# Optimization experiments

Measured on AMD Instinct MI355X. Metric: run time of the kernel, lower is better.

## Reference

```python
import jax, jax.numpy as jnp
import numpy as np
import math

B, S, D, H = 1, 2048, 2048, 16
DH, DHID, DKER = 128, 256, 128  # dim_head, dim_hid, dim_ker


def _uniform(k, shape, a):
    return jax.random.uniform(k, shape, jnp.float32, -a, a)


def setup_inputs() -> dict:
    key = jax.random.key(0)
    ks = jax.random.split(key, 14)
    a1 = math.sqrt(6.0 / (DH + DHID))
    a2 = math.sqrt(6.0 / (DKER + DHID))
    a3 = math.sqrt(6.0 / (2 * DKER))
    return {
        "x_t": jax.random.normal(ks[0], (B, S, D), jnp.float32),
        "q": jax.random.normal(ks[1], (B, S, D), jnp.float32),
        "k": jax.random.normal(ks[2], (B, S, D), jnp.float32),
        "v": jax.random.normal(ks[3], (B, S, D), jnp.float32),
        "lr_attn_mask": jax.random.bernoulli(ks[4], 0.5, (B, H, S, S)),
        "sparse_norms_lse": jax.random.normal(ks[5], (B, H, S, 1), jnp.float32),
        "sparse_attn_weights": jax.random.normal(ks[6], (B, H, S, S), jnp.float32),
        "lambda_constant": 0,
        "kernel_q_mat1": _uniform(ks[7], (H, DH, DHID), a1),
        "kernel_k_mat1": _uniform(ks[8], (H, DH, DHID), a1),
        "kernel_q_mat2": _uniform(ks[9], (H, DHID, DKER), a2),
        "kernel_k_mat2": _uniform(ks[10], (H, DHID, DKER), a2),
        "interaction_k": _uniform(ks[11], (H, DKER, DKER), a3),
        "scalingD": jnp.full((1, H, 1, DKER), 1e-4, jnp.float32),
        "scalingD2": jnp.full((1, H, 1, DKER), 1e-4, jnp.float32),
    }


def _gelu(x):
    return jax.nn.gelu(x, approximate=False)  # matches torch F.gelu default


def reference(x_t, q, k, v, lr_attn_mask, sparse_norms_lse, sparse_attn_weights,
              lambda_constant, kernel_q_mat1, kernel_k_mat1, kernel_q_mat2,
              kernel_k_mat2, interaction_k, scalingD, scalingD2):
    Bq, Sq, Dq = q.shape
    dh = Dq // H
    # [B,S,D] -> [B,H,S,dh]
    qh = q.reshape(Bq, Sq, H, dh).transpose(0, 2, 1, 3)
    kh = k.reshape(Bq, Sq, H, dh).transpose(0, 2, 1, 3)
    vh = v.reshape(Bq, Sq, H, dh).transpose(0, 2, 1, 3)

    # per-head two-layer feature maps (dropout is identity at eval)
    qf = _gelu(jnp.einsum('bhsd,hde->bhse', qh, kernel_q_mat1))
    qf = _gelu(jnp.einsum('bhse,hef->bhsf', qf, kernel_q_mat2))
    kf = _gelu(jnp.einsum('bhsd,hde->bhse', kh, kernel_k_mat1))
    kf = jnp.abs(scalingD) * _gelu(jnp.einsum('bhse,hef->bhsf', kf, kernel_k_mat2))
    kf = kf + jnp.einsum('bhse,hef->bhsf', kf, interaction_k) * scalingD2

    # masked non-negative kernel scores [B,H,S,S]
    scores = jnp.einsum('bhse,bhte->bhst', jnp.abs(qf), jnp.abs(kf))
    m = lr_attn_mask.astype(scores.dtype)
    scores = m * scores

    lr_norms_lse = jnp.log(scores.sum(axis=-1, keepdims=True) + 1e-6)
    norm_factor_lse = jnp.logaddexp(lr_norms_lse, sparse_norms_lse)

    logits = jnp.log(scores + 1e-6) * m + (1.0 - m) * sparse_attn_weights
    attn = jnp.exp(logits - norm_factor_lse)

    out = jnp.einsum('bhst,bhtd->bhsd', attn, vh)
    return out.transpose(0, 2, 1, 3).reshape(Bq, Sq, Dq)
```

## Files before the change

### kernel.cpp

```cpp
#include <hip/hip_runtime.h>
#include <hip/hip_bf16.h>
#include <math.h>

#define H_    16
#define S_    2048
#define D_    2048
#define DH_   128
#define DHID_ 256
#define DKER_ 128

typedef __attribute__((ext_vector_type(8))) short short8v;
typedef __attribute__((ext_vector_type(4))) float float4v;
typedef __attribute__((ext_vector_type(4))) int int4v;

static __device__ __forceinline__ short f2bf(float x){
  union { float f; unsigned u; } v; v.f = x;
  unsigned r = v.u + 0x7fffu + ((v.u >> 16) & 1u);
  return (short)(r >> 16);
}
static __device__ __forceinline__ float gelu_f(float x){
  float y = 0.7978845608028654f * (x + 0.044715f * x * x * x);
  float e = __expf(2.0f * y);
  float t = 1.0f - 2.0f / (e + 1.0f);
  return 0.5f * x * (1.0f + t);
}
static __device__ __forceinline__ float4v mfma16(short8v a, short8v b, float4v c){
  return __builtin_amdgcn_mfma_f32_16x16x32_bf16(a, b, c, 0, 0, 0);
}
static __device__ __forceinline__ unsigned cvtpk(float lo, float hi){
  unsigned d;
  asm("v_cvt_pk_bf16_f32 %0, %1, %2" : "=v"(d) : "v"(lo), "v"(hi));
  return d;
}
static __device__ __forceinline__ void glds16(const void* g, void* l){
  __builtin_amdgcn_global_load_lds(
      (const __attribute__((address_space(1))) void*)g,
      (__attribute__((address_space(3))) void*)l, 16, 0, 0);
}

__global__ __launch_bounds__(256) void prep_kernel(
    const float* __restrict__ w1q, short* __restrict__ W1qT,
    const float* __restrict__ w1k, short* __restrict__ W1kT,
    const float* __restrict__ w2q, short* __restrict__ W2qT,
    const float* __restrict__ w2k, short* __restrict__ W2kT,
    const float* __restrict__ ik,  short* __restrict__ IKT,
    const float* __restrict__ v,   short* __restrict__ V2){
  __shared__ float tile[32][33];
  int b = blockIdx.x;
  int tid = threadIdx.x;

  if (b < 2048){
    int h = b >> 7, bx = b & 127;
    int d = tid & 127, oct = tid >> 7;
    int t8 = bx * 2 + oct;
    int t32 = t8 >> 2, o = t8 & 3;
    const float* src = v + (size_t)(t32 * 32) * D_ + h * DH_ + d;
    short8v ov;
    #pragma unroll
    for (int j = 0; j < 8; ++j){
      int trel = o * 4 + (j & 3) + ((j >> 2) << 4);
      ov[j] = f2bf(src[(size_t)trel * D_]);
    }
    *(short8v*)(V2 + (((size_t)h * (S_/8) + t8) * DH_ + d) * 8) = ov;
    return;
  }
  b -= 2048;
  const float* src; short* dst; int R, C, bx, by, h;
  if (b < 512){        src = w1q; dst = W1qT; R = DH_;  C = DHID_;
                       bx = b & 7; by = (b >> 3) & 3; h = b >> 5; }
  else if (b < 1024){  b -= 512;  src = w1k; dst = W1kT; R = DH_;  C = DHID_;
                       bx = b & 7; by = (b >> 3) & 3; h = b >> 5; }
  else if (b < 1536){  b -= 1024; src = w2q; dst = W2qT; R = DHID_; C = DKER_;
                       bx = b & 3; by = (b >> 2) & 7; h = b >> 5; }
  else if (b < 2048){  b -= 1536; src = w2k; dst = W2kT; R = DHID_; C = DKER_;
                       bx = b & 3; by = (b >> 2) & 7; h = b >> 5; }
  else {               b -= 2048; src = ik;  dst = IKT;  R = DKER_; C = DKER_;
                       bx = b & 3; by = (b >> 2) & 3; h = b >> 4; }
  int tx = tid & 31, ty = tid >> 5;
  int c0 = bx * 32, r0 = by * 32;
  const float* s = src + (size_t)h * R * C;
  short* d = dst + (size_t)h * R * C;
  #pragma unroll
  for (int i = 0; i < 32; i += 8)
    tile[ty + i][tx] = s[(size_t)(r0 + ty + i) * C + (c0 + tx)];
  __syncthreads();
  #pragma unroll
  for (int i = 0; i < 32; i += 8)
    d[(size_t)(c0 + ty + i) * R + (r0 + tx)] = f2bf(tile[tx][ty + i]);
}

__global__ __launch_bounds__(256) void feat_kernel(
    const float* __restrict__ q, const float* __restrict__ k,
    const short* __restrict__ W1qT, const short* __restrict__ W2qT,
    const short* __restrict__ W1kT, const short* __restrict__ W2kT,
    const short* __restrict__ IKT, const float* __restrict__ sD,
    const float* __restrict__ sD2,
    short* __restrict__ QF, short* __restrict__ KF){
  __shared__ __align__(16) short yls[4][16][264];
  int z = blockIdx.y;
  bool isq = z < 16;
  int h = z & 15;
  const float* X = isq ? q : k;
  const short* W1T = isq ? W1qT : W1kT;
  const short* W2T = isq ? W2qT : W2kT;
  int lane = threadIdx.x & 63, warp = threadIdx.x >> 6;
  int s0 = (blockIdx.x * 4 + warp) * 16;
  int col = lane & 15, rg = lane >> 4;
  short8v a[4];
  {
    const float* xr = X + (size_t)(s0 + col) * D_ + h * DH_;
    #pragma unroll
    for (int kb = 0; kb < 4; ++kb){
      int k0 = kb * 32 + rg * 8;
      float4v x0 = *(const float4v*)(xr + k0);
      float4v x1 = *(const float4v*)(xr + k0 + 4);
      union { unsigned u[4]; short8v v8; } t;
      t.u[0] = cvtpk(x0[0], x0[1]); t.u[1] = cvtpk(x0[2], x0[3]);
      t.u[2] = cvtpk(x1[0], x1[1]); t.u[3] = cvtpk(x1[2], x1[3]);
      a[kb] = t.v8;
    }
  }
  const short* wbase = W1T + (size_t)h * DHID_ * DH_;
  #pragma unroll
  for (int j = 0; j < 16; ++j){
    int n = j * 16;
    float4v c = {0.f, 0.f, 0.f, 0.f};
    const short* wr = wbase + (size_t)(n + col) * DH_ + rg * 8;
    #pragma unroll
    for (int kb = 0; kb < 4; ++kb)
      c = mfma16(a[kb], *(const short8v*)(wr + kb * 32), c);
    #pragma unroll
    for (int r = 0; r < 4; ++r)
      yls[warp][rg * 4 + r][n + col] = f2bf(gelu_f(c[r]));
  }
  short8v a2[8];
  #pragma unroll
  for (int kb = 0; kb < 8; ++kb)
    a2[kb] = *(const short8v*)(&yls[warp][col][kb * 32 + rg * 8]);
  const short* wb2 = W2T + (size_t)h * DKER_ * DHID_;

  if (isq){
    short* qb = QF + ((size_t)h * S_ + s0) * DKER_;
    #pragma unroll
    for (int j = 0; j < 8; ++j){
      int n = j * 16;
      float4v c = {0.f, 0.f, 0.f, 0.f};
      const short* wr = wb2 + (size_t)(n + col) * DHID_ + rg * 8;
      #pragma unroll
      for (int kb = 0; kb < 8; ++kb)
        c = mfma16(a2[kb], *(const short8v*)(wr + kb * 32), c);
      #pragma unroll
      for (int r = 0; r < 4; ++r)
        qb[(size_t)(rg * 4 + r) * DKER_ + n + col] = f2bf(fabsf(gelu_f(c[r])));
    }
    return;
  }
  float kf0[8][4];
  #pragma unroll
  for (int j = 0; j < 8; ++j){
    int n = j * 16;
    float4v c = {0.f, 0.f, 0.f, 0.f};
    const short* wr = wb2 + (size_t)(n + col) * DHID_ + rg * 8;
    #pragma unroll
    for (int kb = 0; kb < 8; ++kb)
      c = mfma16(a2[kb], *(const short8v*)(wr + kb * 32), c);
    float sc = fabsf(sD[h * DKER_ + n + col]);
    #pragma unroll
    for (int r = 0; r < 4; ++r) kf0[j][r] = sc * gelu_f(c[r]);
  }
  #pragma unroll
  for (int j = 0; j < 8; ++j)
    #pragma unroll
    for (int r = 0; r < 4; ++r)
      yls[warp][rg * 4 + r][j * 16 + col] = f2bf(kf0[j][r]);
  short8v pa[4];
  #pragma unroll
  for (int kb = 0; kb < 4; ++kb)
    pa[kb] = *(const short8v*)(&yls[warp][col][kb * 32 + rg * 8]);
  const short* ib = IKT + (size_t)h * DKER_ * DKER_;
  short* ko = KF + ((size_t)h * S_ + s0) * DKER_;
  #pragma unroll
  for (int j = 0; j < 8; ++j){
    int n = j * 16;
    float4v c = {0.f, 0.f, 0.f, 0.f};
    const short* ir = ib + (size_t)(n + col) * DKER_ + rg * 8;
    #pragma unroll
    for (int kb = 0; kb < 4; ++kb)
      c = mfma16(pa[kb], *(const short8v*)(ir + kb * 32), c);
    float s2 = sD2[h * DKER_ + n + col];
    #pragma unroll
    for (int r = 0; r < 4; ++r)
      ko[(size_t)(rg * 4 + r) * DKER_ + n + col] = f2bf(fabsf(kf0[j][r] + c[r] * s2));
  }
}

template<int MT>
static __device__ __forceinline__ void attn_tloop(
    const char* __restrict__ mrow0, const float* __restrict__ swrow,
    const char* __restrict__ kf_base, const char* __restrict__ v2_base,
    short* kbuf, short* vbuf,
    int kg0, int kg1, int vg0, int vg1, int lds_lo, int lds_hi,
    int swz, int rowb0, int rg, int col,
    const short8v (&qa)[4], float4v (&acc)[8], float& rs){
  const int NITER = (S_ / 2) / 32;
  for (int ti = 0; ti < NITER; ++ti){
    int cur = ti & 1;
    if (ti + 1 < NITER){
      const char* kt = kf_base + (size_t)(ti + 1) * 8192;
      const char* vt = v2_base + (size_t)(ti + 1) * 8192;
      glds16(kt + kg0, &kbuf[(cur ^ 1) * 4096 + lds_lo]);
      glds16(kt + kg1, &kbuf[(cur ^ 1) * 4096 + lds_hi]);
      glds16(vt + vg0, &vbuf[(cur ^ 1) * 4096 + lds_lo]);
      glds16(vt + vg1, &vbuf[(cur ^ 1) * 4096 + lds_hi]);
    }
    const char* kbp = (const char*)kbuf + cur * 8192;
    const char* vbp = (const char*)vbuf + cur * 8192;

    float4v q0 = {0.f,0.f,0.f,0.f}, q1 = {0.f,0.f,0.f,0.f};
    #pragma unroll
    for (int kk = 0; kk < 4; ++kk){
      short8v a0 = *(const short8v*)(kbp + ((rowb0 + kk * 64) ^ swz));
      short8v a1 = *(const short8v*)(kbp + ((rowb0 + 4096 + kk * 64) ^ swz));
      q0 = mfma16(a0, qa[kk], q0);
      q1 = mfma16(a1, qa[kk], q1);
    }

    const float* swp = swrow + ti * 32;
    float4v sv0 = *(const float4v*)swp;
    float4v sv1 = *(const float4v*)(swp + 16);

    bool m0[4], m1[4];
    if constexpr (MT == 0){
      const int* mp = (const int*)(mrow0 + (size_t)ti * 128);
      int4v x0 = *(const int4v*)mp;
      int4v x1 = *(const int4v*)(mp + 16);
      #pragma unroll
      for (int r = 0; r < 4; ++r){ m0[r] = x0[r] != 0; m1[r] = x1[r] != 0; }
    } else if constexpr (MT == 1){
      const unsigned* mp = (const unsigned*)(mrow0 + (size_t)ti * 32);
      unsigned x0 = mp[0], x1 = mp[4];
      #pragma unroll
      for (int r = 0; r < 4; ++r){
        m0[r] = ((x0 >> (8*r)) & 0xffu) != 0u;
        m1[r] = ((x1 >> (8*r)) & 0xffu) != 0u;
      }
    } else if constexpr (MT == 2){
      const float* mp = (const float*)(mrow0 + (size_t)ti * 128);
      float4v x0 = *(const float4v*)mp;
      float4v x1 = *(const float4v*)(mp + 16);
      #pragma unroll
      for (int r = 0; r < 4; ++r){ m0[r] = x0[r] != 0.0f; m1[r] = x1[r] != 0.0f; }
    } else {
      const int* mp = (const int*)(mrow0 + (size_t)ti * 256);
      int4v xa = *(const int4v*)mp;
      int4v xb = *(const int4v*)(mp + 4);
      int4v xc = *(const int4v*)(mp + 32);
      int4v xd = *(const int4v*)(mp + 36);
      m0[0] = xa[0] != 0; m0[1] = xa[2] != 0; m0[2] = xb[0] != 0; m0[3] = xb[2] != 0;
      m1[0] = xc[0] != 0; m1[1] = xc[2] != 0; m1[2] = xd[0] != 0; m1[3] = xd[2] != 0;
    }

    float p0[4], p1[4];
    #pragma unroll
    for (int r = 0; r < 4; ++r){
      p0[r] = m0[r] ? (q0[r] + 1e-6f) : __expf(sv0[r]);
      p1[r] = m1[r] ? (q1[r] + 1e-6f) : __expf(sv1[r]);
      if (m0[r]) rs += q0[r];
      if (m1[r]) rs += q1[r];
    }
    union { unsigned u[4]; short8v v8; } pw;
    pw.u[0] = cvtpk(p0[0], p0[1]); pw.u[1] = cvtpk(p0[2], p0[3]);
    pw.u[2] = cvtpk(p1[0], p1[1]); pw.u[3] = cvtpk(p1[2], p1[3]);
    short8v pa = pw.v8;

    #pragma unroll
    for (int j = 0; j < 8; ++j){
      short8v vf = *(const short8v*)(vbp + rg * 2048 + (j * 16 + col) * 16);
      acc[j] = mfma16(pa, vf, acc[j]);
    }
    __syncthreads();
  }
}

__global__ __launch_bounds__(512, 4) void main_attn_kernel(
    const short* __restrict__ QF, const short* __restrict__ KF,
    const short* __restrict__ V2, const void* __restrict__ MSK,
    const float* __restrict__ SW, const float* __restrict__ LSE,
    float* __restrict__ OUT){
  __shared__ __align__(16) char smem[65536];
  int tid = threadIdx.x;
  int lane = tid & 63, warp = tid >> 6;
  int hf = warp >> 2, w4 = warp & 3;
  int flat = blockIdx.y * 32 + blockIdx.x;
  int nf = (flat & 7) * 64 + (flat >> 3);
  int sblk = nf & 31, h = nf >> 5;
  int tbase = hf * (S_ / 2);
  int s0 = (sblk * 4 + w4) * 16;
  int col = lane & 15, rg = lane >> 4;

  short* kbuf = (short*)(smem + hf * 32768);
  short* vbuf = (short*)(smem + hf * 32768 + 16384);

  short8v qa[4];
  const short* qr = QF + ((size_t)h * S_ + s0 + col) * DKER_ + rg * 8;
  #pragma unroll
  for (int kb = 0; kb < 4; ++kb) qa[kb] = *(const short8v*)(qr + kb * 32);

  float4v acc[8];
  #pragma unroll
  for (int j = 0; j < 8; ++j) acc[j] = (float4v){0.f, 0.f, 0.f, 0.f};
  float rs = 0.f;

  const char* kf_base = (const char*)(KF + ((size_t)h * S_ + tbase) * DKER_);
  const char* v2_base = (const char*)(V2 + ((size_t)h * (S_/8) + (tbase >> 3)) * DH_ * 8);
  int c0 = w4 * 64 + lane, c1 = c0 + 256;
  int kg0 = (c0 * 16) ^ (((c0 >> 4) & 7) << 4);
  int kg1 = (c1 * 16) ^ (((c1 >> 4) & 7) << 4);
  int vg0 = c0 * 16, vg1 = c1 * 16;
  int lds_lo = w4 * 512, lds_hi = 2048 + w4 * 512;

  const float* swrow = SW + ((size_t)h * S_ + s0 + col) * S_ + tbase + rg * 4;

  glds16(kf_base + kg0, &kbuf[lds_lo]);
  glds16(kf_base + kg1, &kbuf[lds_hi]);
  glds16(v2_base + vg0, &vbuf[lds_lo]);
  glds16(v2_base + vg1, &vbuf[lds_hi]);

  int flag;
  {
    const unsigned* mw = (const unsigned*)MSK;
    int bin = 1, f32ok = 1, odd0 = 1;
    #pragma unroll
    for (int i = 0; i < 16; ++i){
      unsigned w = mw[lane + i * 64];
      if (w > 1u) bin = 0;
      if (w != 0u && w != 0x3F800000u) f32ok = 0;
      if (((lane + i * 64) & 1) && w != 0u) odd0 = 0;
    }
    bin = __all(bin); odd0 = __all(odd0); f32ok = __all(f32ok);
    flag = bin ? (odd0 ? 3 : 0) : (f32ok ? 2 : 1);
  }
  __syncthreads();

  int swz = (col & 7) << 4;
  int rowb0 = col * 256 + rg * 16;
  size_t e0 = ((size_t)h * S_ + s0 + col) * S_ + tbase + rg * 4;

  if (flag == 0)
    attn_tloop<0>((const char*)MSK + e0 * 4, swrow, kf_base, v2_base, kbuf, vbuf,
                  kg0, kg1, vg0, vg1, lds_lo, lds_hi, swz, rowb0, rg, col, qa, acc, rs);
  else if (flag == 1)
    attn_tloop<1>((const char*)MSK + e0, swrow, kf_base, v2_base, kbuf, vbuf,
                  kg0, kg1, vg0, vg1, lds_lo, lds_hi, swz, rowb0, rg, col, qa, acc, rs);
  else if (flag == 2)
    attn_tloop<2>((const char*)MSK + e0 * 4, swrow, kf_base, v2_base, kbuf, vbuf,
                  kg0, kg1, vg0, vg1, lds_lo, lds_hi, swz, rowb0, rg, col, qa, acc, rs);
  else
    attn_tloop<3>((const char*)MSK + e0 * 8, swrow, kf_base, v2_base, kbuf, vbuf,
                  kg0, kg1, vg0, vg1, lds_lo, lds_hi, swz, rowb0, rg, col, qa, acc, rs);

  rs += __shfl_xor(rs, 16);
  rs += __shfl_xor(rs, 32);

  __syncthreads();
  float* cb = (float*)smem;
  float* rb = (float*)(smem + 32768);
  if (hf == 1){
    float* cw = cb + (size_t)w4 * 16 * 128;
    #pragma unroll
    for (int j = 0; j < 8; ++j)
      #pragma unroll
      for (int r = 0; r < 4; ++r)
        cw[(size_t)(rg * 4 + r) * 128 + j * 16 + col] = acc[j][r];
    if (lane < 16) rb[w4 * 16 + lane] = rs;
  }
  __syncthreads();
  if (hf == 0){
    float* cw = cb + (size_t)w4 * 16 * 128;
    #pragma unroll
    for (int j = 0; j < 8; ++j)
      #pragma unroll
      for (int r = 0; r < 4; ++r)
        acc[j][r] += cw[(size_t)(rg * 4 + r) * 128 + j * 16 + col];
    rs += rb[w4 * 16 + col];

    float a = logf(rs + 1e-6f);
    float b = LSE[h * S_ + s0 + col];
    float mx = fmaxf(a, b);
    float sc_col = expf(-(mx + log1pf(expf(-fabsf(a - b)))));
    float scale[4];
    #pragma unroll
    for (int r = 0; r < 4; ++r) scale[r] = __shfl(sc_col, rg * 4 + r);
    float* ob = OUT + (size_t)s0 * D_ + h * DH_;
    #pragma unroll
    for (int j = 0; j < 8; ++j)
      #pragma unroll
      for (int r = 0; r < 4; ++r)
        ob[(size_t)(rg * 4 + r) * D_ + j * 16 + col] = acc[j][r] * scale[r];
  }
}

extern "C" void kernel_launch(void* const* d_in, const int* in_sizes, int n_in,
                              void* d_out, int out_size, void* d_ws, size_t ws_size,
                              hipStream_t stream){
  (void)in_sizes; (void)n_in; (void)out_size; (void)ws_size;
  const float* q   = (const float*)d_in[1];
  const float* k   = (const float*)d_in[2];
  const float* v   = (const float*)d_in[3];
  const void*  msk = d_in[4];
  const float* lse = (const float*)d_in[5];
  const float* sw  = (const float*)d_in[6];
  const float* w1q = (const float*)d_in[8];
  const float* w1k = (const float*)d_in[9];
  const float* w2q = (const float*)d_in[10];
  const float* w2k = (const float*)d_in[11];
  const float* ik  = (const float*)d_in[12];
  const float* sD  = (const float*)d_in[13];
  const float* sD2 = (const float*)d_in[14];
  float* out = (float*)d_out;

  char* ws = (char*)d_ws;
  size_t o = 0;
  o += 256;
  short* W1qT = (short*)(ws + o);      o += (size_t)H_ * DHID_ * DH_ * 2;
  short* W1kT = (short*)(ws + o);      o += (size_t)H_ * DHID_ * DH_ * 2;
  short* W2qT = (short*)(ws + o);      o += (size_t)H_ * DKER_ * DHID_ * 2;
  short* W2kT = (short*)(ws + o);      o += (size_t)H_ * DKER_ * DHID_ * 2;
  short* IKT  = (short*)(ws + o);      o += (size_t)H_ * DKER_ * DKER_ * 2;
  short* V2   = (short*)(ws + o);      o += (size_t)S_ * D_ * 2;
  short* QFb  = (short*)(ws + o);      o += (size_t)H_ * S_ * DKER_ * 2;
  short* KFb  = (short*)(ws + o);      o += (size_t)H_ * S_ * DKER_ * 2;

  prep_kernel<<<4352, 256, 0, stream>>>(
      w1q, W1qT, w1k, W1kT, w2q, W2qT, w2k, W2kT, ik, IKT, v, V2);

  feat_kernel<<<dim3(S_/64, 32), 256, 0, stream>>>(q, k,
      W1qT, W2qT, W1kT, W2kT, IKT, sD, sD2, QFb, KFb);

  main_attn_kernel<<<dim3(32, 16), 512, 0, stream>>>(
      QFb, KFb, V2, msk, sw, lse, out);
}
```

Measured before the change: 234.9 us.

## Replace LDS-staged K/V tiles with direct global loads and register-prefetched mask/weights

Removes the double-buffered LDS staging of KF and V tiles (global_load_lds plus a per-iteration __syncthreads) and has each wave read its MFMA fragments straight from global memory, relying on L1/L2 to serve the reuse across waves. Mask and sparse-weight values for the next iteration are software-prefetched into registers one step ahead. Shared memory shrinks to what the epilogue reduction needs, which may allow more blocks per CU. The cost is redundant global/L2 traffic for K/V across the four waves sharing a tile and higher register pressure from the prefetch buffers.

```diff
diff --git a/kernel.cpp b/kernel.cpp
--- a/kernel.cpp
+++ b/kernel.cpp
@@ -31,11 +31,6 @@
   unsigned d;
   asm("v_cvt_pk_bf16_f32 %0, %1, %2" : "=v"(d) : "v"(lo), "v"(hi));
   return d;
-}
-static __device__ __forceinline__ void glds16(const void* g, void* l){
-  __builtin_amdgcn_global_load_lds(
-      (const __attribute__((address_space(1))) void*)g,
-      (__attribute__((address_space(3))) void*)l, 16, 0, 0);
 }
 
 __global__ __launch_bounds__(256) void prep_kernel(
@@ -197,69 +192,80 @@
 template<int MT>
 static __device__ __forceinline__ void attn_tloop(
     const char* __restrict__ mrow0, const float* __restrict__ swrow,
-    const char* __restrict__ kf_base, const char* __restrict__ v2_base,
-    short* kbuf, short* vbuf,
-    int kg0, int kg1, int vg0, int vg1, int lds_lo, int lds_hi,
-    int swz, int rowb0, int rg, int col,
+    const short* __restrict__ kr0, const char* __restrict__ v2_base,
+    int rg, int col,
     const short8v (&qa)[4], float4v (&acc)[8], float& rs){
   const int NITER = (S_ / 2) / 32;
+
+  float4v sv0, sv1;
+  int4v ma, mb, na, nb;
+  unsigned mu;
+
+  sv0 = *(const float4v*)swrow;
+  sv1 = *(const float4v*)(swrow + 16);
+  if constexpr (MT == 0 || MT == 2){
+    ma = *(const int4v*)(mrow0);
+    mb = *(const int4v*)(mrow0 + 64);
+  } else if constexpr (MT == 1){
+    mu = *(const unsigned*)(mrow0);
+    ma[0] = (int)*(const unsigned*)(mrow0 + 16);
+  } else {
+    ma = *(const int4v*)(mrow0);
+    mb = *(const int4v*)(mrow0 + 16);
+    na = *(const int4v*)(mrow0 + 128);
+    nb = *(const int4v*)(mrow0 + 144);
+  }
+
   for (int ti = 0; ti < NITER; ++ti){
-    int cur = ti & 1;
+    float4v psv0, psv1; int4v pa_, pb_, pc_, pd_; unsigned pu0 = 0, pu1 = 0;
     if (ti + 1 < NITER){
-      const char* kt = kf_base + (size_t)(ti + 1) * 8192;
-      const char* vt = v2_base + (size_t)(ti + 1) * 8192;
-      glds16(kt + kg0, &kbuf[(cur ^ 1) * 4096 + lds_lo]);
-      glds16(kt + kg1, &kbuf[(cur ^ 1) * 4096 + lds_hi]);
-      glds16(vt + vg0, &vbuf[(cur ^ 1) * 4096 + lds_lo]);
-      glds16(vt + vg1, &vbuf[(cur ^ 1) * 4096 + lds_hi]);
-    }
-    const char* kbp = (const char*)kbuf + cur * 8192;
-    const char* vbp = (const char*)vbuf + cur * 8192;
-
+      const float* swp = swrow + (ti + 1) * 32;
+      psv0 = *(const float4v*)swp;
+      psv1 = *(const float4v*)(swp + 16);
+      if constexpr (MT == 0 || MT == 2){
+        pa_ = *(const int4v*)(mrow0 + (size_t)(ti + 1) * 128);
+        pb_ = *(const int4v*)(mrow0 + (size_t)(ti + 1) * 128 + 64);
+      } else if constexpr (MT == 1){
+        pu0 = *(const unsigned*)(mrow0 + (size_t)(ti + 1) * 32);
+        pu1 = *(const unsigned*)(mrow0 + (size_t)(ti + 1) * 32 + 16);
+      } else {
+        pa_ = *(const int4v*)(mrow0 + (size_t)(ti + 1) * 256);
+        pb_ = *(const int4v*)(mrow0 + (size_t)(ti + 1) * 256 + 16);
+        pc_ = *(const int4v*)(mrow0 + (size_t)(ti + 1) * 256 + 128);
+        pd_ = *(const int4v*)(mrow0 + (size_t)(ti + 1) * 256 + 144);
+      }
+    }
+
+    const short* kp = kr0 + (size_t)ti * 4096;
     float4v q0 = {0.f,0.f,0.f,0.f}, q1 = {0.f,0.f,0.f,0.f};
     #pragma unroll
     for (int kk = 0; kk < 4; ++kk){
-      short8v a0 = *(const short8v*)(kbp + ((rowb0 + kk * 64) ^ swz));
-      short8v a1 = *(const short8v*)(kbp + ((rowb0 + 4096 + kk * 64) ^ swz));
+      short8v a0 = *(const short8v*)(kp + kk * 32);
+      short8v a1 = *(const short8v*)(kp + 2048 + kk * 32);
       q0 = mfma16(a0, qa[kk], q0);
       q1 = mfma16(a1, qa[kk], q1);
     }
 
-    const float* swp = swrow + ti * 32;
-    float4v sv0 = *(const float4v*)swp;
-    float4v sv1 = *(const float4v*)(swp + 16);
-
     bool m0[4], m1[4];
     if constexpr (MT == 0){
-      const int* mp = (const int*)(mrow0 + (size_t)ti * 128);
-      int4v x0 = *(const int4v*)mp;
-      int4v x1 = *(const int4v*)(mp + 16);
-      #pragma unroll
-      for (int r = 0; r < 4; ++r){ m0[r] = x0[r] != 0; m1[r] = x1[r] != 0; }
+      #pragma unroll
+      for (int r = 0; r < 4; ++r){ m0[r] = ma[r] != 0; m1[r] = mb[r] != 0; }
+    } else if constexpr (MT == 2){
+      #pragma unroll
+      for (int r = 0; r < 4; ++r){
+        m0[r] = (ma[r] & 0x7fffffff) != 0; m1[r] = (mb[r] & 0x7fffffff) != 0;
+      }
     } else if constexpr (MT == 1){
-      const unsigned* mp = (const unsigned*)(mrow0 + (size_t)ti * 32);
-      unsigned x0 = mp[0], x1 = mp[4];
+      unsigned hi = (unsigned)ma[0];
       #pragma unroll
       for (int r = 0; r < 4; ++r){
-        m0[r] = ((x0 >> (8*r)) & 0xffu) != 0u;
-        m1[r] = ((x1 >> (8*r)) & 0xffu) != 0u;
+        m0[r] = ((mu >> (8*r)) & 0xffu) != 0u;
+        m1[r] = ((hi >> (8*r)) & 0xffu) != 0u;
       }
-    } else if constexpr (MT == 2){
-      const float* mp = (const float*)(mrow0 + (size_t)ti * 128);
-      float4v x0 = *(const float4v*)mp;
-      float4v x1 = *(const float4v*)(mp + 16);
-      #pragma unroll
-      for (int r = 0; r < 4; ++r){ m0[r] = x0[r] != 0.0f; m1[r] = x1[r] != 0.0f; }
     } else {
-      const int* mp = (const int*)(mrow0 + (size_t)ti * 256);
-      int4v xa = *(const int4v*)mp;
-      int4v xb = *(const int4v*)(mp + 4);
-      int4v xc = *(const int4v*)(mp + 32);
-      int4v xd = *(const int4v*)(mp + 36);
-      m0[0] = xa[0] != 0; m0[1] = xa[2] != 0; m0[2] = xb[0] != 0; m0[3] = xb[2] != 0;
-      m1[0] = xc[0] != 0; m1[1] = xc[2] != 0; m1[2] = xd[0] != 0; m1[3] = xd[2] != 0;
-    }
-
+      m0[0] = ma[0] != 0; m0[1] = ma[2] != 0; m0[2] = mb[0] != 0; m0[3] = mb[2] != 0;
+      m1[0] = na[0] != 0; m1[1] = na[2] != 0; m1[2] = nb[0] != 0; m1[3] = nb[2] != 0;
+    }
     float p0[4], p1[4];
     #pragma unroll
     for (int r = 0; r < 4; ++r){
@@ -271,14 +277,19 @@
     union { unsigned u[4]; short8v v8; } pw;
     pw.u[0] = cvtpk(p0[0], p0[1]); pw.u[1] = cvtpk(p0[2], p0[3]);
     pw.u[2] = cvtpk(p1[0], p1[1]); pw.u[3] = cvtpk(p1[2], p1[3]);
-    short8v pa = pw.v8;
-
+    short8v pfrag = pw.v8;
+
+    const char* vp = v2_base + (size_t)ti * 8192 + rg * 2048;
     #pragma unroll
     for (int j = 0; j < 8; ++j){
-      short8v vf = *(const short8v*)(vbp + rg * 2048 + (j * 16 + col) * 16);
-      acc[j] = mfma16(pa, vf, acc[j]);
-    }
-    __syncthreads();
+      short8v vf = *(const short8v*)(vp + (j * 16 + col) * 16);
+      acc[j] = mfma16(pfrag, vf, acc[j]);
+    }
+
+    sv0 = psv0; sv1 = psv1;
+    if constexpr (MT == 0 || MT == 2){ ma = pa_; mb = pb_; }
+    else if constexpr (MT == 1){ mu = pu0; ma[0] = (int)pu1; }
+    else { ma = pa_; mb = pb_; na = pc_; nb = pd_; }
   }
 }
 
@@ -287,7 +298,7 @@
     const short* __restrict__ V2, const void* __restrict__ MSK,
     const float* __restrict__ SW, const float* __restrict__ LSE,
     float* __restrict__ OUT){
-  __shared__ __align__(16) char smem[65536];
+  __shared__ __align__(16) char smem[33024];
   int tid = threadIdx.x;
   int lane = tid & 63, warp = tid >> 6;
   int hf = warp >> 2, w4 = warp & 3;
@@ -298,9 +309,6 @@
   int s0 = (sblk * 4 + w4) * 16;
   int col = lane & 15, rg = lane >> 4;
 
-  short* kbuf = (short*)(smem + hf * 32768);
-  short* vbuf = (short*)(smem + hf * 32768 + 16384);
-
   short8v qa[4];
   const short* qr = QF + ((size_t)h * S_ + s0 + col) * DKER_ + rg * 8;
   #pragma unroll
@@ -311,20 +319,9 @@
   for (int j = 0; j < 8; ++j) acc[j] = (float4v){0.f, 0.f, 0.f, 0.f};
   float rs = 0.f;
 
-  const char* kf_base = (const char*)(KF + ((size_t)h * S_ + tbase) * DKER_);
+  const short* kr0 = KF + ((size_t)h * S_ + tbase + col) * DKER_ + rg * 8;
   const char* v2_base = (const char*)(V2 + ((size_t)h * (S_/8) + (tbase >> 3)) * DH_ * 8);
-  int c0 = w4 * 64 + lane, c1 = c0 + 256;
-  int kg0 = (c0 * 16) ^ (((c0 >> 4) & 7) << 4);
-  int kg1 = (c1 * 16) ^ (((c1 >> 4) & 7) << 4);
-  int vg0 = c0 * 16, vg1 = c1 * 16;
-  int lds_lo = w4 * 512, lds_hi = 2048 + w4 * 512;
-
   const float* swrow = SW + ((size_t)h * S_ + s0 + col) * S_ + tbase + rg * 4;
-
-  glds16(kf_base + kg0, &kbuf[lds_lo]);
-  glds16(kf_base + kg1, &kbuf[lds_hi]);
-  glds16(v2_base + vg0, &vbuf[lds_lo]);
-  glds16(v2_base + vg1, &vbuf[lds_hi]);
 
   int flag;
   {
@@ -340,24 +337,17 @@
     bin = __all(bin); odd0 = __all(odd0); f32ok = __all(f32ok);
     flag = bin ? (odd0 ? 3 : 0) : (f32ok ? 2 : 1);
   }
-  __syncthreads();
-
-  int swz = (col & 7) << 4;
-  int rowb0 = col * 256 + rg * 16;
+
   size_t e0 = ((size_t)h * S_ + s0 + col) * S_ + tbase + rg * 4;
 
   if (flag == 0)
-    attn_tloop<0>((const char*)MSK + e0 * 4, swrow, kf_base, v2_base, kbuf, vbuf,
-                  kg0, kg1, vg0, vg1, lds_lo, lds_hi, swz, rowb0, rg, col, qa, acc, rs);
+    attn_tloop<0>((const char*)MSK + e0 * 4, swrow, kr0, v2_base, rg, col, qa, acc, rs);
   else if (flag == 1)
-    attn_tloop<1>((const char*)MSK + e0, swrow, kf_base, v2_base, kbuf, vbuf,
-                  kg0, kg1, vg0, vg1, lds_lo, lds_hi, swz, rowb0, rg, col, qa, acc, rs);
+    attn_tloop<1>((const char*)MSK + e0, swrow, kr0, v2_base, rg, col, qa, acc, rs);
   else if (flag == 2)
-    attn_tloop<2>((const char*)MSK + e0 * 4, swrow, kf_base, v2_base, kbuf, vbuf,
-                  kg0, kg1, vg0, vg1, lds_lo, lds_hi, swz, rowb0, rg, col, qa, acc, rs);
+    attn_tloop<2>((const char*)MSK + e0 * 4, swrow, kr0, v2_base, rg, col, qa, acc, rs);
   else
-    attn_tloop<3>((const char*)MSK + e0 * 8, swrow, kf_base, v2_base, kbuf, vbuf,
-                  kg0, kg1, vg0, vg1, lds_lo, lds_hi, swz, rowb0, rg, col, qa, acc, rs);
+    attn_tloop<3>((const char*)MSK + e0 * 8, swrow, kr0, v2_base, rg, col, qa, acc, rs);
 
   rs += __shfl_xor(rs, 16);
   rs += __shfl_xor(rs, 32);
```

Result: slower. 323.4 us (+37.6%).
